# Kernel tuning notes

Hardware: AMD Instinct MI355X
Metric: run time of the kernel (lower is better)

Reference implementation:

```python
import jax, jax.numpy as jnp
import numpy as np

# binarize = sign() in forward; standard BNN binarize uses a straight-through
# estimator (gradient clipped to |x|<=1) in backward. Forward math: sign.

def binarize(x):
    return jnp.sign(x)


def setup_inputs() -> dict:
    key = jax.random.key(0)
    k1, k2 = jax.random.split(key)
    M, K, N = 8192, 4096, 4096
    x = jax.random.normal(k1, (M, K), dtype=jnp.float32)
    # xavier-scale init for weight; scale is irrelevant after sign() but kept realistic
    w = jax.random.normal(k2, (K, N), dtype=jnp.float32) * np.sqrt(2.0 / (K + N)).astype(np.float32)
    return {"x": x, "weight": w}


def reference(x, weight):
    # sign-binarize activations and weights, then dense matmul
    xb = binarize(x)            # [M, K] in {-1, 0, +1}
    wb = binarize(weight)       # [K, N]
    return jnp.matmul(xb, wb)   # [M, N]
```

## Files before the change

kernel.cpp:

```cpp
#include <hip/hip_runtime.h>
#include <stdint.h>

#define M_DIM 8192
#define K_DIM 4096
#define N_DIM 4096
#define KB2 2048

using i32x4 = __attribute__((ext_vector_type(4))) int;
using i32x8 = __attribute__((ext_vector_type(8))) int;
using f32x16 = __attribute__((ext_vector_type(16))) float;

typedef const __attribute__((address_space(1))) void g_void;
typedef __attribute__((address_space(3))) void lds_void;

__device__ __forceinline__ void gload_lds16(const void* g, void* l) {
  __builtin_amdgcn_global_load_lds((g_void*)g, (lds_void*)l, 16, 0, 0);
}

__device__ __forceinline__ void barrier_raw() {
  asm volatile("" ::: "memory");
  __builtin_amdgcn_s_barrier();
  asm volatile("" ::: "memory");
}

__device__ __forceinline__ unsigned code4(float v) {
  return v > 0.f ? 0x2u : (v < 0.f ? 0xAu : 0x0u);
}

__global__ void pack_x4_kernel(const float* __restrict__ in,
                               unsigned* __restrict__ out, long n8) {
  long i0 = (long)blockIdx.x * blockDim.x + threadIdx.x;
  long stride = (long)gridDim.x * blockDim.x;
  for (long i = i0; i < n8; i += stride) {
    const float4* p = reinterpret_cast<const float4*>(in + i * 8);
    float4 x0 = p[0], x1 = p[1];
    unsigned w = code4(x0.x) | (code4(x0.y) << 4) | (code4(x0.z) << 8) |
                 (code4(x0.w) << 12) | (code4(x1.x) << 16) |
                 (code4(x1.y) << 20) | (code4(x1.z) << 24) |
                 (code4(x1.w) << 28);
    out[i] = w;
  }
}

__global__ void pack_wt4_kernel(const float* __restrict__ w,
                                unsigned* __restrict__ wt4) {
  __shared__ uint8_t tile[64 * 68];
  int n0 = blockIdx.x * 64;
  int k0 = blockIdx.y * 64;
  int t = threadIdx.x;
#pragma unroll
  for (int i = 0; i < 16; ++i) {
    int flat = t + 256 * i;
    int r = flat >> 6;
    int c = flat & 63;
    tile[c * 68 + r] = (uint8_t)code4(w[(long)(k0 + r) * N_DIM + n0 + c]);
  }
  __syncthreads();
#pragma unroll
  for (int i = 0; i < 2; ++i) {
    int flat = t + 256 * i;
    int nn = flat >> 3;
    int dk = flat & 7;
    const uint8_t* src = &tile[nn * 68 + dk * 8];
    unsigned word = 0;
#pragma unroll
    for (int e = 0; e < 8; ++e) word |= ((unsigned)src[e]) << (4 * e);
    wt4[(long)(n0 + nn) * (K_DIM / 8) + (k0 >> 3) + dk] = word;
  }
}

__device__ __forceinline__ i32x8 lo8(i32x4 r) {
  return __builtin_shufflevector(r, r, 0, 1, 2, 3, -1, -1, -1, -1);
}

#define SCALE1 0x7f7f7f7f

template <int VM, bool ISSUE>
__device__ __forceinline__ void tile_step(
    int t, const uint8_t* __restrict__ Asrc, const uint8_t* __restrict__ Bsrc,
    long off0, long off1, int dstOff, uint8_t* lds, int aRd, int bRd,
    f32x16 (&acc)[4][2]) {
  const uint8_t* buf = lds + (t & 3) * 32768;
  if (ISSUE) {
    long kn = (long)(t + 3) * 64;
    uint8_t* nbuf = lds + ((t + 3) & 3) * 32768;
    gload_lds16(Asrc + off0 + kn, nbuf + dstOff);
    gload_lds16(Asrc + off1 + kn, nbuf + 8192 + dstOff);
    gload_lds16(Bsrc + off0 + kn, nbuf + 16384 + dstOff);
    gload_lds16(Bsrc + off1 + kn, nbuf + 24576 + dstOff);
  }
  i32x4 a0[4], b0[2], a1[4], b1[2];
#pragma unroll
  for (int mi = 0; mi < 4; ++mi)
    a0[mi] = *reinterpret_cast<const i32x4*>(buf + aRd + mi * 2048);
#pragma unroll
  for (int ni = 0; ni < 2; ++ni)
    b0[ni] = *reinterpret_cast<const i32x4*>(buf + bRd + ni * 2048);
#pragma unroll
  for (int mi = 0; mi < 4; ++mi)
    a1[mi] = *reinterpret_cast<const i32x4*>(buf + aRd + mi * 2048 + 1024);
#pragma unroll
  for (int ni = 0; ni < 2; ++ni)
    b1[ni] = *reinterpret_cast<const i32x4*>(buf + bRd + ni * 2048 + 1024);
  asm volatile("s_waitcnt lgkmcnt(6)" ::: "memory");
  __builtin_amdgcn_sched_barrier(0);
  __builtin_amdgcn_s_setprio(1);
#pragma unroll
  for (int mi = 0; mi < 4; ++mi)
#pragma unroll
    for (int ni = 0; ni < 2; ++ni)
      acc[mi][ni] = __builtin_amdgcn_mfma_scale_f32_32x32x64_f8f6f4(
          lo8(a0[mi]), lo8(b0[ni]), acc[mi][ni], 4, 4, 0, SCALE1, 0, SCALE1);
  __builtin_amdgcn_s_setprio(0);
  asm volatile("s_waitcnt lgkmcnt(0)" ::: "memory");
  __builtin_amdgcn_sched_barrier(0);
  __builtin_amdgcn_s_setprio(1);
#pragma unroll
  for (int mi = 0; mi < 4; ++mi)
#pragma unroll
    for (int ni = 0; ni < 2; ++ni)
      acc[mi][ni] = __builtin_amdgcn_mfma_scale_f32_32x32x64_f8f6f4(
          lo8(a1[mi]), lo8(b1[ni]), acc[mi][ni], 4, 4, 0, SCALE1, 0, SCALE1);
  __builtin_amdgcn_s_setprio(0);
  if (VM >= 0) {
    if (VM == 8) asm volatile("s_waitcnt vmcnt(8)" ::: "memory");
    else if (VM == 4) asm volatile("s_waitcnt vmcnt(4)" ::: "memory");
    else asm volatile("s_waitcnt vmcnt(0)" ::: "memory");
    barrier_raw();
  }
}

__global__ __launch_bounds__(512, 2) void gemm_fp4_kernel(
    const uint8_t* __restrict__ A, const uint8_t* __restrict__ B,
    float* __restrict__ C) {
  __shared__ __align__(16) uint8_t lds[4 * 32768];

  int bid = blockIdx.x;
  int xcd = bid & 7;
  int i = bid >> 3;
  int bn = (i & 7) + ((xcd & 1) << 3);
  int bm = (i >> 3) + ((xcd >> 1) << 3);

  int tid = threadIdx.x;
  int wid = tid >> 6;
  int lane = tid & 63;
  int wr = wid >> 2;
  int wc = wid & 3;

  const uint8_t* Asrc = A + (long)bm * 256 * KB2;
  const uint8_t* Bsrc = B + (long)bn * 256 * KB2;

  long off0 = (long)((tid >> 7) * 32 + (tid & 31)) * KB2 + (((tid >> 5) & 3) << 4);
  long off1 = off0 + 128L * KB2;
  int dstOff = wid * 1024;

  int aRd = (wr * 4) * 2048 + lane * 16;
  int bRd = 16384 + (wc * 2) * 2048 + lane * 16;

  f32x16 acc[4][2] = {};

#pragma unroll
  for (int t = 0; t < 3; ++t) {
    uint8_t* buf = lds + t * 32768;
    long k0 = (long)t * 64;
    gload_lds16(Asrc + off0 + k0, buf + dstOff);
    gload_lds16(Asrc + off1 + k0, buf + 8192 + dstOff);
    gload_lds16(Bsrc + off0 + k0, buf + 16384 + dstOff);
    gload_lds16(Bsrc + off1 + k0, buf + 24576 + dstOff);
  }
  asm volatile("s_waitcnt vmcnt(8)" ::: "memory");
  barrier_raw();

#pragma unroll 1
  for (int t = 0; t < 29; ++t)
    tile_step<8, true>(t, Asrc, Bsrc, off0, off1, dstOff, lds, aRd, bRd, acc);
  tile_step<4, false>(29, Asrc, Bsrc, off0, off1, dstOff, lds, aRd, bRd, acc);
  tile_step<0, false>(30, Asrc, Bsrc, off0, off1, dstOff, lds, aRd, bRd, acc);
  tile_step<-1, false>(31, Asrc, Bsrc, off0, off1, dstOff, lds, aRd, bRd, acc);

  long row0 = (long)bm * 256 + wr * 128 + ((lane >> 5) << 2);
  long col0 = (long)bn * 256 + wc * 64 + (lane & 31);
#pragma unroll
  for (int mi = 0; mi < 4; ++mi)
#pragma unroll
    for (int ni = 0; ni < 2; ++ni)
#pragma unroll
      for (int r = 0; r < 16; ++r) {
        long row = row0 + mi * 32 + (r & 3) + ((r >> 2) << 3);
        C[row * N_DIM + col0 + ni * 32] = acc[mi][ni][r];
      }
}

extern "C" void kernel_launch(void* const* d_in, const int* in_sizes, int n_in,
                              void* d_out, int out_size, void* d_ws, size_t ws_size,
                              hipStream_t stream) {
  const float* x = (const float*)d_in[0];
  const float* w = (const float*)d_in[1];
  float* out = (float*)d_out;

  uint8_t* x4 = (uint8_t*)d_ws;
  uint8_t* w4t = x4 + (size_t)M_DIM * KB2;

  pack_x4_kernel<<<2048, 256, 0, stream>>>(x, (unsigned*)x4,
                                           (long)M_DIM * K_DIM / 8);
  pack_wt4_kernel<<<dim3(N_DIM / 64, K_DIM / 64), 256, 0, stream>>>(
      w, (unsigned*)w4t);
  gemm_fp4_kernel<<<512, 512, 0, stream>>>(x4, w4t, out);
}
```

Measured before the change: 141.3 us.

## Interleave LDS reads, global prefetch and MFMAs in barrier-synchronized phases

Restructures each k-step into four phases. Each phase loads a small set of LDS fragments, issues one global-to-LDS prefetch, then runs four MFMAs, with workgroup barriers between phases. The aim is to spread memory traffic across the MFMA stream and lower register pressure by holding fewer fragments at once. In exchange it adds eight barriers per k-step and fully waits on LDS before each MFMA group, which can serialize execution across waves.

```diff
diff --git a/kernel.cpp b/kernel.cpp
--- a/kernel.cpp
+++ b/kernel.cpp
@@ -75,59 +75,64 @@
 
 #define SCALE1 0x7f7f7f7f
 
+#define MFMA4(ACCI)                                                        \
+  do {                                                                     \
+    asm volatile("s_waitcnt lgkmcnt(0)" ::: "memory");                     \
+    __builtin_amdgcn_sched_barrier(0);                                     \
+    __builtin_amdgcn_s_setprio(1);                                         \
+    acc[ACCI][0] = __builtin_amdgcn_mfma_scale_f32_32x32x64_f8f6f4(        \
+        lo8(a[0]), lo8(b[0]), acc[ACCI][0], 4, 4, 0, SCALE1, 0, SCALE1);   \
+    acc[ACCI][1] = __builtin_amdgcn_mfma_scale_f32_32x32x64_f8f6f4(        \
+        lo8(a[0]), lo8(b[1]), acc[ACCI][1], 4, 4, 0, SCALE1, 0, SCALE1);   \
+    acc[ACCI + 1][0] = __builtin_amdgcn_mfma_scale_f32_32x32x64_f8f6f4(    \
+        lo8(a[1]), lo8(b[0]), acc[ACCI + 1][0], 4, 4, 0, SCALE1, 0,        \
+        SCALE1);                                                           \
+    acc[ACCI + 1][1] = __builtin_amdgcn_mfma_scale_f32_32x32x64_f8f6f4(    \
+        lo8(a[1]), lo8(b[1]), acc[ACCI + 1][1], 4, 4, 0, SCALE1, 0,        \
+        SCALE1);                                                           \
+    __builtin_amdgcn_s_setprio(0);                                         \
+  } while (0)
+
 template <int VM, bool ISSUE>
 __device__ __forceinline__ void tile_step(
     int t, const uint8_t* __restrict__ Asrc, const uint8_t* __restrict__ Bsrc,
     long off0, long off1, int dstOff, uint8_t* lds, int aRd, int bRd,
     f32x16 (&acc)[4][2]) {
   const uint8_t* buf = lds + (t & 3) * 32768;
-  if (ISSUE) {
-    long kn = (long)(t + 3) * 64;
-    uint8_t* nbuf = lds + ((t + 3) & 3) * 32768;
-    gload_lds16(Asrc + off0 + kn, nbuf + dstOff);
-    gload_lds16(Asrc + off1 + kn, nbuf + 8192 + dstOff);
-    gload_lds16(Bsrc + off0 + kn, nbuf + 16384 + dstOff);
-    gload_lds16(Bsrc + off1 + kn, nbuf + 24576 + dstOff);
-  }
-  i32x4 a0[4], b0[2], a1[4], b1[2];
-#pragma unroll
-  for (int mi = 0; mi < 4; ++mi)
-    a0[mi] = *reinterpret_cast<const i32x4*>(buf + aRd + mi * 2048);
-#pragma unroll
-  for (int ni = 0; ni < 2; ++ni)
-    b0[ni] = *reinterpret_cast<const i32x4*>(buf + bRd + ni * 2048);
-#pragma unroll
-  for (int mi = 0; mi < 4; ++mi)
-    a1[mi] = *reinterpret_cast<const i32x4*>(buf + aRd + mi * 2048 + 1024);
-#pragma unroll
-  for (int ni = 0; ni < 2; ++ni)
-    b1[ni] = *reinterpret_cast<const i32x4*>(buf + bRd + ni * 2048 + 1024);
-  asm volatile("s_waitcnt lgkmcnt(6)" ::: "memory");
-  __builtin_amdgcn_sched_barrier(0);
-  __builtin_amdgcn_s_setprio(1);
-#pragma unroll
-  for (int mi = 0; mi < 4; ++mi)
-#pragma unroll
-    for (int ni = 0; ni < 2; ++ni)
-      acc[mi][ni] = __builtin_amdgcn_mfma_scale_f32_32x32x64_f8f6f4(
-          lo8(a0[mi]), lo8(b0[ni]), acc[mi][ni], 4, 4, 0, SCALE1, 0, SCALE1);
-  __builtin_amdgcn_s_setprio(0);
-  asm volatile("s_waitcnt lgkmcnt(0)" ::: "memory");
-  __builtin_amdgcn_sched_barrier(0);
-  __builtin_amdgcn_s_setprio(1);
-#pragma unroll
-  for (int mi = 0; mi < 4; ++mi)
-#pragma unroll
-    for (int ni = 0; ni < 2; ++ni)
-      acc[mi][ni] = __builtin_amdgcn_mfma_scale_f32_32x32x64_f8f6f4(
-          lo8(a1[mi]), lo8(b1[ni]), acc[mi][ni], 4, 4, 0, SCALE1, 0, SCALE1);
-  __builtin_amdgcn_s_setprio(0);
-  if (VM >= 0) {
-    if (VM == 8) asm volatile("s_waitcnt vmcnt(8)" ::: "memory");
-    else if (VM == 4) asm volatile("s_waitcnt vmcnt(4)" ::: "memory");
-    else asm volatile("s_waitcnt vmcnt(0)" ::: "memory");
-    barrier_raw();
-  }
+  uint8_t* nbuf = lds + ((t + 3) & 3) * 32768;
+  long kn = (long)(t + 3) * 64;
+  i32x4 a[2], b[2];
+  a[0] = *reinterpret_cast<const i32x4*>(buf + aRd);
+  a[1] = *reinterpret_cast<const i32x4*>(buf + aRd + 2048);
+  b[0] = *reinterpret_cast<const i32x4*>(buf + bRd);
+  b[1] = *reinterpret_cast<const i32x4*>(buf + bRd + 2048);
+  if (ISSUE) gload_lds16(Asrc + off0 + kn, nbuf + dstOff);
+  barrier_raw();
+  MFMA4(0);
+  barrier_raw();
+  a[0] = *reinterpret_cast<const i32x4*>(buf + aRd + 2 * 2048);
+  a[1] = *reinterpret_cast<const i32x4*>(buf + aRd + 3 * 2048);
+  if (ISSUE) gload_lds16(Asrc + off1 + kn, nbuf + 8192 + dstOff);
+  barrier_raw();
+  MFMA4(2);
+  barrier_raw();
+  a[0] = *reinterpret_cast<const i32x4*>(buf + aRd + 1024);
+  a[1] = *reinterpret_cast<const i32x4*>(buf + aRd + 2048 + 1024);
+  b[0] = *reinterpret_cast<const i32x4*>(buf + bRd + 1024);
+  b[1] = *reinterpret_cast<const i32x4*>(buf + bRd + 2048 + 1024);
+  if (ISSUE) gload_lds16(Bsrc + off0 + kn, nbuf + 16384 + dstOff);
+  barrier_raw();
+  MFMA4(0);
+  barrier_raw();
+  a[0] = *reinterpret_cast<const i32x4*>(buf + aRd + 2 * 2048 + 1024);
+  a[1] = *reinterpret_cast<const i32x4*>(buf + aRd + 3 * 2048 + 1024);
+  if (ISSUE) gload_lds16(Bsrc + off1 + kn, nbuf + 24576 + dstOff);
+  if (VM == 8) asm volatile("s_waitcnt vmcnt(8)" ::: "memory");
+  else if (VM == 4) asm volatile("s_waitcnt vmcnt(4)" ::: "memory");
+  else if (VM == 0) asm volatile("s_waitcnt vmcnt(0)" ::: "memory");
+  barrier_raw();
+  MFMA4(2);
+  barrier_raw();
 }
 
 __global__ __launch_bounds__(512, 2) void gemm_fp4_kernel(
```

Result: no change. 141.0 us (-0.3%).

## Pre-tile packed FP4 operands so GEMM loads contiguous 2KB chunks per wave

Applied to the files above, without the earlier changes.

The packing kernels now write the FP4 activations and transposed weights in a tiled layout: per 32-row group, per 128-wide K tile, four 16-byte K chunks across 32 rows. Each GEMM wave can then fetch its LDS tile slice with two fully contiguous 1KB global_load_lds requests, instead of strided row reads spread across 2KB-pitch rows. This is meant to cut DRAM/L2 transaction scattering in the main loop. The cost is more complex pack kernels that stage through LDS, which add their own transpose and shuffle work.

```diff
diff --git a/kernel.cpp b/kernel.cpp
--- a/kernel.cpp
+++ b/kernel.cpp
@@ -4,7 +4,6 @@
 #define M_DIM 8192
 #define K_DIM 4096
 #define N_DIM 4096
-#define KB2 2048
 
 using i32x4 = __attribute__((ext_vector_type(4))) int;
 using i32x8 = __attribute__((ext_vector_type(8))) int;
@@ -28,45 +27,68 @@
 }
 
 __global__ void pack_x4_kernel(const float* __restrict__ in,
-                               unsigned* __restrict__ out, long n8) {
-  long i0 = (long)blockIdx.x * blockDim.x + threadIdx.x;
-  long stride = (long)gridDim.x * blockDim.x;
-  for (long i = i0; i < n8; i += stride) {
-    const float4* p = reinterpret_cast<const float4*>(in + i * 8);
-    float4 x0 = p[0], x1 = p[1];
-    unsigned w = code4(x0.x) | (code4(x0.y) << 4) | (code4(x0.z) << 8) |
-                 (code4(x0.w) << 12) | (code4(x1.x) << 16) |
-                 (code4(x1.y) << 20) | (code4(x1.z) << 24) |
-                 (code4(x1.w) << 28);
-    out[i] = w;
+                               uint8_t* __restrict__ out) {
+  __shared__ __align__(16) uint16_t cds[32 * 264];
+  int g = blockIdx.x;
+  int tq = blockIdx.y;
+  int tid = threadIdx.x;
+#pragma unroll
+  for (int i = 0; i < 32; ++i) {
+    int flat = tid + 256 * i;
+    int row = flat >> 8;
+    int c4 = flat & 255;
+    const float4 v = *reinterpret_cast<const float4*>(
+        in + (long)(g * 32 + row) * K_DIM + tq * 1024 + c4 * 4);
+    unsigned u = code4(v.x) | (code4(v.y) << 4) | (code4(v.z) << 8) |
+                 (code4(v.w) << 12);
+    cds[row * 264 + c4] = (uint16_t)u;
+  }
+  __syncthreads();
+#pragma unroll
+  for (int j = 0; j < 4; ++j) {
+    int u = tid + 256 * j;
+    int tl = u >> 7;
+    int kc = (u >> 5) & 3;
+    int row = u & 31;
+    i32x4 val = *reinterpret_cast<const i32x4*>(
+        &cds[row * 264 + tl * 32 + kc * 8]);
+    int t = tq * 8 + tl;
+    long o = ((((long)g * 32 + t) * 4 + kc) * 32 + row) * 16;
+    *reinterpret_cast<i32x4*>(out + o) = val;
   }
 }
 
 __global__ void pack_wt4_kernel(const float* __restrict__ w,
-                                unsigned* __restrict__ wt4) {
-  __shared__ uint8_t tile[64 * 68];
+                                uint8_t* __restrict__ out) {
+  __shared__ __align__(16) uint8_t tile[64 * 144];
   int n0 = blockIdx.x * 64;
-  int k0 = blockIdx.y * 64;
-  int t = threadIdx.x;
-#pragma unroll
-  for (int i = 0; i < 16; ++i) {
-    int flat = t + 256 * i;
+  int k0 = blockIdx.y * 128;
+  int tid = threadIdx.x;
+#pragma unroll
+  for (int i = 0; i < 32; ++i) {
+    int flat = tid + 256 * i;
     int r = flat >> 6;
     int c = flat & 63;
-    tile[c * 68 + r] = (uint8_t)code4(w[(long)(k0 + r) * N_DIM + n0 + c]);
+    tile[c * 144 + r] = (uint8_t)code4(w[(long)(k0 + r) * N_DIM + n0 + c]);
   }
   __syncthreads();
-#pragma unroll
-  for (int i = 0; i < 2; ++i) {
-    int flat = t + 256 * i;
-    int nn = flat >> 3;
-    int dk = flat & 7;
-    const uint8_t* src = &tile[nn * 68 + dk * 8];
-    unsigned word = 0;
-#pragma unroll
-    for (int e = 0; e < 8; ++e) word |= ((unsigned)src[e]) << (4 * e);
-    wt4[(long)(n0 + nn) * (K_DIM / 8) + (k0 >> 3) + dk] = word;
-  }
+  int rg = tid >> 7, kc = (tid >> 5) & 3, row = tid & 31;
+  const unsigned* sp =
+      reinterpret_cast<const unsigned*>(&tile[(rg * 32 + row) * 144 + kc * 32]);
+  i32x4 val;
+#pragma unroll
+  for (int d = 0; d < 4; ++d) {
+    unsigned s0 = sp[2 * d], s1 = sp[2 * d + 1];
+    unsigned t0 = s0 & 0x0F0F0F0Fu, t1 = s1 & 0x0F0F0F0Fu;
+    unsigned p = (t0 | (t0 >> 4)) & 0x00FF00FFu;
+    unsigned q = (t1 | (t1 >> 4)) & 0x00FF00FFu;
+    val[d] = (int)((p & 0xFFu) | ((p >> 8) & 0xFF00u) | ((q & 0xFFu) << 16) |
+                   ((q >> 16) << 24));
+  }
+  int g = (n0 >> 5) + rg;
+  int t = k0 >> 7;
+  long o = ((((long)g * 32 + t) * 4 + kc) * 32 + row) * 16;
+  *reinterpret_cast<i32x4*>(out + o) = val;
 }
 
 __device__ __forceinline__ i32x8 lo8(i32x4 r) {
@@ -77,17 +99,16 @@
 
 template <int VM, bool ISSUE>
 __device__ __forceinline__ void tile_step(
-    int t, const uint8_t* __restrict__ Asrc, const uint8_t* __restrict__ Bsrc,
-    long off0, long off1, int dstOff, uint8_t* lds, int aRd, int bRd,
-    f32x16 (&acc)[4][2]) {
+    int t, const uint8_t* __restrict__ gA, const uint8_t* __restrict__ gB,
+    int dstA, int dstB, uint8_t* lds, int aRd, int bRd, f32x16 (&acc)[4][2]) {
   const uint8_t* buf = lds + (t & 3) * 32768;
   if (ISSUE) {
-    long kn = (long)(t + 3) * 64;
+    long kn = (long)(t + 3) * 2048;
     uint8_t* nbuf = lds + ((t + 3) & 3) * 32768;
-    gload_lds16(Asrc + off0 + kn, nbuf + dstOff);
-    gload_lds16(Asrc + off1 + kn, nbuf + 8192 + dstOff);
-    gload_lds16(Bsrc + off0 + kn, nbuf + 16384 + dstOff);
-    gload_lds16(Bsrc + off1 + kn, nbuf + 24576 + dstOff);
+    gload_lds16(gA + kn, nbuf + dstA);
+    gload_lds16(gA + kn + 1024, nbuf + dstA + 1024);
+    gload_lds16(gB + kn, nbuf + dstB);
+    gload_lds16(gB + kn + 1024, nbuf + dstB + 1024);
   }
   i32x4 a0[4], b0[2], a1[4], b1[2];
 #pragma unroll
@@ -147,12 +168,10 @@
   int wr = wid >> 2;
   int wc = wid & 3;
 
-  const uint8_t* Asrc = A + (long)bm * 256 * KB2;
-  const uint8_t* Bsrc = B + (long)bn * 256 * KB2;
-
-  long off0 = (long)((tid >> 7) * 32 + (tid & 31)) * KB2 + (((tid >> 5) & 3) << 4);
-  long off1 = off0 + 128L * KB2;
-  int dstOff = wid * 1024;
+  const uint8_t* gA = A + (long)(bm * 8 + wid) * 32 * 2048 + lane * 16;
+  const uint8_t* gB = B + (long)(bn * 8 + wid) * 32 * 2048 + lane * 16;
+  int dstA = wid * 2048;
+  int dstB = 16384 + wid * 2048;
 
   int aRd = (wr * 4) * 2048 + lane * 16;
   int bRd = 16384 + (wc * 2) * 2048 + lane * 16;
@@ -162,21 +181,21 @@
 #pragma unroll
   for (int t = 0; t < 3; ++t) {
     uint8_t* buf = lds + t * 32768;
-    long k0 = (long)t * 64;
-    gload_lds16(Asrc + off0 + k0, buf + dstOff);
-    gload_lds16(Asrc + off1 + k0, buf + 8192 + dstOff);
-    gload_lds16(Bsrc + off0 + k0, buf + 16384 + dstOff);
-    gload_lds16(Bsrc + off1 + k0, buf + 24576 + dstOff);
+    long k0 = (long)t * 2048;
+    gload_lds16(gA + k0, buf + dstA);
+    gload_lds16(gA + k0 + 1024, buf + dstA + 1024);
+    gload_lds16(gB + k0, buf + dstB);
+    gload_lds16(gB + k0 + 1024, buf + dstB + 1024);
   }
   asm volatile("s_waitcnt vmcnt(8)" ::: "memory");
   barrier_raw();
 
 #pragma unroll 1
   for (int t = 0; t < 29; ++t)
-    tile_step<8, true>(t, Asrc, Bsrc, off0, off1, dstOff, lds, aRd, bRd, acc);
-  tile_step<4, false>(29, Asrc, Bsrc, off0, off1, dstOff, lds, aRd, bRd, acc);
-  tile_step<0, false>(30, Asrc, Bsrc, off0, off1, dstOff, lds, aRd, bRd, acc);
-  tile_step<-1, false>(31, Asrc, Bsrc, off0, off1, dstOff, lds, aRd, bRd, acc);
+    tile_step<8, true>(t, gA, gB, dstA, dstB, lds, aRd, bRd, acc);
+  tile_step<4, false>(29, gA, gB, dstA, dstB, lds, aRd, bRd, acc);
+  tile_step<0, false>(30, gA, gB, dstA, dstB, lds, aRd, bRd, acc);
+  tile_step<-1, false>(31, gA, gB, dstA, dstB, lds, aRd, bRd, acc);
 
   long row0 = (long)bm * 256 + wr * 128 + ((lane >> 5) << 2);
   long col0 = (long)bn * 256 + wc * 64 + (lane & 31);
@@ -199,11 +218,9 @@
   float* out = (float*)d_out;
 
   uint8_t* x4 = (uint8_t*)d_ws;
-  uint8_t* w4t = x4 + (size_t)M_DIM * KB2;
-
-  pack_x4_kernel<<<2048, 256, 0, stream>>>(x, (unsigned*)x4,
-                                           (long)M_DIM * K_DIM / 8);
-  pack_wt4_kernel<<<dim3(N_DIM / 64, K_DIM / 64), 256, 0, stream>>>(
-      w, (unsigned*)w4t);
+  uint8_t* w4t = x4 + (size_t)M_DIM * (K_DIM / 2);
+
+  pack_x4_kernel<<<dim3(M_DIM / 32, 4), 256, 0, stream>>>(x, x4);
+  pack_wt4_kernel<<<dim3(N_DIM / 64, K_DIM / 128), 256, 0, stream>>>(w, w4t);
   gemm_fp4_kernel<<<512, 512, 0, stream>>>(x4, w4t, out);
 }
```

Measured after the change: 132.1 us. 6.5% less time.
